# Optimization experiments

Hardware: AMD Instinct MI355X
Metric: run time of the kernel (lower is better)

## Reference

```python
import jax, jax.numpy as jnp
import numpy as np

D_MODEL = 1024
N_HEADS = 16
D_K = D_MODEL // N_HEADS
THETA = 10000.0
SEQ = 2048
BATCH = 2


def setup_inputs() -> dict:
    key = jax.random.key(0)
    ks = jax.random.split(key, 5)
    std = (2.0 / (D_MODEL + D_MODEL)) ** 0.5
    return {
        "x": jax.random.normal(ks[0], (BATCH, SEQ, D_MODEL), dtype=jnp.float32),
        "token_positions": jnp.arange(SEQ, dtype=jnp.int64 if jax.config.jax_enable_x64 else jnp.int32),
        "wq": jax.random.normal(ks[1], (D_MODEL, D_MODEL), dtype=jnp.float32) * std,
        "wk": jax.random.normal(ks[2], (D_MODEL, D_MODEL), dtype=jnp.float32) * std,
        "wv": jax.random.normal(ks[3], (D_MODEL, D_MODEL), dtype=jnp.float32) * std,
        "wo": jax.random.normal(ks[4], (D_MODEL, D_MODEL), dtype=jnp.float32) * std,
    }


def _apply_rope(t, token_positions):
    # t: [b, h, s, d_k]; interleaved even/odd rotation (RoPE)
    k = jnp.arange(D_K // 2, dtype=t.dtype)
    inv_freq = THETA ** (-2.0 * k / D_K)                     # [d_k/2]
    angles = token_positions.astype(t.dtype)[:, None] * inv_freq  # [s, d_k/2]
    cos, sin = jnp.cos(angles), jnp.sin(angles)
    even, odd = t[..., 0::2], t[..., 1::2]
    re = even * cos - odd * sin
    ro = odd * cos + even * sin
    # re-interleave: stack last then reshape back to [..., d_k]
    return jnp.stack([re, ro], axis=-1).reshape(t.shape)


def reference(x, token_positions, wq, wk, wv, wo):
    b, s, _ = x.shape
    def proj(w):
        y = jnp.einsum("bsd,ed->bse", x, w)               # Linear: x @ W^T
        return y.reshape(b, s, N_HEADS, D_K).transpose(0, 2, 1, 3)  # [b,h,s,dk]
    q, k, v = proj(wq), proj(wk), proj(wv)
    q = _apply_rope(q, token_positions)
    k = _apply_rope(k, token_positions)
    scores = jnp.einsum("bhqd,bhkd->bhqk", q, k) / jnp.sqrt(jnp.asarray(D_K, x.dtype))
    attn = jax.nn.softmax(scores, axis=-1)
    out = jnp.einsum("bhqk,bhkd->bhqd", attn, v)          # [b,h,s,dk]
    out = out.transpose(0, 2, 1, 3).reshape(b, s, D_MODEL)
    return jnp.einsum("bsd,ed->bse", out, wo)
```

## Files before the change

### kernel.cpp

```cpp
#include <hip/hip_runtime.h>
#include <stdint.h>

typedef __bf16 bf16x8 __attribute__((ext_vector_type(8)));
typedef __bf16 bf16x2 __attribute__((ext_vector_type(2)));
typedef float f32x4 __attribute__((ext_vector_type(4)));
typedef float f32x16 __attribute__((ext_vector_type(16)));
typedef unsigned short ushort_t;
typedef unsigned int uint;

#define SEQ    2048
#define DMODEL 1024
#define NHEAD  16
#define DKH    64
#define NBATCH 2
#define MROWS  (NBATCH*SEQ)
#define LOG2E  1.44269504088896340736f

__device__ __forceinline__ uint pk2(float a, float b) {
  bf16x2 t; t[0] = (__bf16)a; t[1] = (__bf16)b;
  return __builtin_bit_cast(uint, t);
}
__device__ __forceinline__ ushort_t b1(float a) {
  return __builtin_bit_cast(ushort_t, (__bf16)a);
}
__device__ __forceinline__ float fexp2(float x) {
#if __has_builtin(__builtin_amdgcn_exp2f)
  return __builtin_amdgcn_exp2f(x);
#else
  return exp2f(x);
#endif
}

__device__ __forceinline__ void gload16(const void* g, void* l) {
  __builtin_amdgcn_global_load_lds(
      (const __attribute__((address_space(1))) void*)g,
      (__attribute__((address_space(3))) void*)l, 16, 0, 0);
}

__device__ __forceinline__ f32x4 mfma16(bf16x8 a, bf16x8 b, f32x4 c) {
  return __builtin_amdgcn_mfma_f32_16x16x32_bf16(a, b, c, 0, 0, 0);
}
__device__ __forceinline__ f32x16 mfma32(bf16x8 a, bf16x8 b, f32x16 c) {
  return __builtin_amdgcn_mfma_f32_32x32x16_bf16(a, b, c, 0, 0, 0);
}

__global__ __launch_bounds__(256) void cvt_all(
    const float* __restrict__ x, const float* __restrict__ wq,
    const float* __restrict__ wk, const float* __restrict__ wv,
    const float* __restrict__ wo, uint2* __restrict__ out)
{
  int b = blockIdx.x;
  const float4* src; uint2* dst; int i;
  if (b < 4096) {
    i = b * 256 + threadIdx.x; src = (const float4*)x; dst = out;
  } else {
    int s = (b - 4096) >> 10;
    i = ((b - 4096) & 1023) * 256 + threadIdx.x;
    src = (const float4*)(s == 0 ? wq : s == 1 ? wk : s == 2 ? wv : wo);
    dst = out + (size_t)1048576 + (size_t)s * 262144;
  }
  float4 v = src[i];
  uint2 r; r.x = pk2(v.x, v.y); r.y = pk2(v.z, v.w);
  dst[i] = r;
}

__global__ __launch_bounds__(256) void rope_tab_kernel(const int* __restrict__ tokpos, float2* __restrict__ tab) {
  int t = blockIdx.x * 256 + threadIdx.x;
  int s = t >> 5, k = t & 31;
  double inv = pow(10000.0, -(double)(2 * k) / 64.0);
  double ang = (double)tokpos[s] * inv;
  tab[t] = make_float2((float)cos(ang), (float)sin(ang));
}

__global__ __launch_bounds__(256) void gemm_nt(
    const ushort_t* __restrict__ A, const ushort_t* __restrict__ W,
    const float2* __restrict__ tab,
    ushort_t* __restrict__ Qo, ushort_t* __restrict__ Ko, ushort_t* __restrict__ Vo,
    float* __restrict__ outf, int fused)
{
  __shared__ ushort_t lA[2][128 * 64];
  __shared__ ushort_t lB[2][128 * 64];
  const int tid = threadIdx.x;
  const int w = tid >> 6, l = tid & 63, lo = l & 15, hi = l >> 4;
  const int wr = (w >> 1) * 64, wc = (w & 1) * 64;
  const char* Ab = (const char*)A + (size_t)blockIdx.y * 128 * 2048;
  const char* Bb = (const char*)W + (size_t)blockIdx.x * 128 * 2048;
  f32x4 acc[4][4] = {};

  const int o0 = w * 1024 + l * 16;
  const int r0 = o0 >> 7;
  const int us = ((o0 >> 4) & 7) ^ (r0 & 7);
  const char* ap = Ab + (size_t)r0 * 2048 + us * 16;
  const char* bp = Bb + (size_t)r0 * 2048 + us * 16;

  auto stage = [&](char* dA, char* dB, const char* aq, const char* bq) {
    #pragma unroll
    for (int i = 0; i < 4; ++i) {
      gload16(aq + i * 65536, dA + w * 1024 + i * 4096);
      gload16(bq + i * 65536, dB + w * 1024 + i * 4096);
    }
  };
  auto comp = [&](const ushort_t* lAb, const ushort_t* lBb) {
    #pragma unroll
    for (int c = 0; c < 2; ++c) {
      bf16x8 af[4], wf[4];
      #pragma unroll
      for (int m = 0; m < 4; ++m) {
        int row = wr + m * 16 + lo;
        af[m] = *(const bf16x8*)((const char*)lAb + row * 128 + ((c * 64 + hi * 16) ^ ((row & 7) << 4)));
      }
      #pragma unroll
      for (int n = 0; n < 4; ++n) {
        int row = wc + n * 16 + lo;
        wf[n] = *(const bf16x8*)((const char*)lBb + row * 128 + ((c * 64 + hi * 16) ^ ((row & 7) << 4)));
      }
      #pragma unroll
      for (int m = 0; m < 4; ++m)
        #pragma unroll
        for (int n = 0; n < 4; ++n)
          acc[m][n] = mfma16(af[m], wf[n], acc[m][n]);
    }
  };

  stage((char*)lA[0], (char*)lB[0], ap, bp); ap += 128; bp += 128;
  __syncthreads();
  for (int it = 0; it < 16; it += 2) {
    stage((char*)lA[1], (char*)lB[1], ap, bp); ap += 128; bp += 128;
    comp(lA[0], lB[0]);
    __syncthreads();
    if (it + 2 < 16) { stage((char*)lA[0], (char*)lB[0], ap, bp); ap += 128; bp += 128; }
    comp(lA[1], lB[1]);
    __syncthreads();
  }

  const int mode = fused ? (blockIdx.x >> 3) : 3;
  const int colblk = fused ? (blockIdx.x & 7) : blockIdx.x;
  const int rowbase = blockIdx.y * 128 + wr + hi * 4;
  const int colbase = colblk * 128 + wc + lo;

  if (mode == 3) {
    #pragma unroll
    for (int m = 0; m < 4; ++m)
      #pragma unroll
      for (int n = 0; n < 4; ++n) {
        int e = colbase + n * 16;
        #pragma unroll
        for (int r = 0; r < 4; ++r) {
          int row = rowbase + m * 16 + r;
          outf[(size_t)row * 1024 + e] = acc[m][n][r];
        }
      }
    return;
  }
  if (mode == 2) {
    #pragma unroll
    for (int m = 0; m < 4; ++m) {
      int row0 = rowbase + m * 16;
      int b = row0 >> 11, s = row0 & 2047;
      #pragma unroll
      for (int n = 0; n < 4; ++n) {
        int e = colbase + n * 16;
        int h = e >> 6, dk = e & 63;
        uint2 pk;
        pk.x = pk2(acc[m][n][0], acc[m][n][1]);
        pk.y = pk2(acc[m][n][2], acc[m][n][3]);
        *(uint2*)(Vo + ((size_t)((b * NHEAD + h) * DKH + dk) * SEQ + s)) = pk;
      }
    }
    return;
  }
  ushort_t* outb = (mode == 0) ? Qo : Ko;
  const float qscale = (mode == 0) ? (0.125f * LOG2E) : 1.0f;
  #pragma unroll
  for (int m = 0; m < 4; ++m) {
    #pragma unroll
    for (int n = 0; n < 4; ++n) {
      int e = colbase + n * 16;
      int h = e >> 6, dk = e & 63, kf = dk >> 1;
      float sgn = (e & 1) ? 1.0f : -1.0f;
      #pragma unroll
      for (int r = 0; r < 4; ++r) {
        int row = rowbase + m * 16 + r;
        int s = row & 2047, b = row >> 11;
        float2 cs = tab[s * 32 + kf];
        float v = acc[m][n][r];
        float p = __shfl_xor(v, 1, 64);
        float res = (v * cs.x + sgn * p * cs.y) * qscale;
        outb[((size_t)((b * NHEAD + h) * SEQ + s)) * DKH + dk] = b1(res);
      }
    }
  }
}

__global__ __launch_bounds__(256) void attn_fwd(
    const ushort_t* __restrict__ Qg, const ushort_t* __restrict__ Kg,
    const ushort_t* __restrict__ VTg, ushort_t* __restrict__ attn)
{
  __shared__ char lds[49152];
  const int tid = threadIdx.x;
  const int w = tid >> 6, l = tid & 63;
  const int q31 = l & 31, hf = l >> 5, s7 = l & 7;
  const int bh = blockIdx.y;
  const int q0 = blockIdx.x * 128 + w * 32;
  const char* Kb = (const char*)Kg + (size_t)bh * 2048 * 128;
  const char* Vb = (const char*)VTg + (size_t)bh * 64 * 4096;

  bf16x8 qreg[4];
  {
    const ushort_t* qp = Qg + ((size_t)bh * 2048 + q0 + q31) * 64 + hf * 8;
    #pragma unroll
    for (int c = 0; c < 4; ++c) qreg[c] = *(const bf16x8*)(qp + c * 16);
  }

  f32x16 accO[2] = {{0,0,0,0,0,0,0,0,0,0,0,0,0,0,0,0},
                    {0,0,0,0,0,0,0,0,0,0,0,0,0,0,0,0}};
  float lsum = 0.f;

  const char* ra[4];
  #pragma unroll
  for (int c = 0; c < 4; ++c)
    ra[c] = lds + q31 * 128 + ((c * 32 + hf * 16) ^ (s7 << 4));
  const int lPoff = 32768 + w * 4096;
  char* wbase = lds + lPoff + q31 * 128 + hf * 8;

  const int o0 = tid * 16;
  const int r0 = o0 >> 7;
  const int us = ((o0 >> 4) & 7) ^ (r0 & 7);
  const char* kp = Kb + (size_t)r0 * 128 + us * 16;
  const char* vp = Vb + (size_t)r0 * 4096 + us * 16;

  auto stage = [&](char* base, const char* kq, const char* vq) {
    gload16(kq,          base + o0);
    gload16(kq + 4096,   base + 4096 + o0);
    gload16(vq,          base + 8192 + o0);
    gload16(vq + 131072, base + 12288 + o0);
  };

  auto tile = [&](int bo) {
    #pragma unroll
    for (int kb = 0; kb < 2; ++kb) {
      f32x16 s = {0,0,0,0,0,0,0,0,0,0,0,0,0,0,0,0};
      #pragma unroll
      for (int c = 0; c < 4; ++c) {
        bf16x8 kf = *(const bf16x8*)(ra[c] + bo + kb * 4096);
        s = mfma32(kf, qreg[c], s);
      }
      float p[16];
      float ts = 0.f;
      #pragma unroll
      for (int r = 0; r < 16; ++r) { p[r] = fexp2(s[r]); ts += p[r]; }
      lsum += ts;
      #pragma unroll
      for (int g2 = 0; g2 < 4; ++g2) {
        uint2 pk;
        pk.x = pk2(p[g2 * 4 + 0], p[g2 * 4 + 1]);
        pk.y = pk2(p[g2 * 4 + 2], p[g2 * 4 + 3]);
        *(uint2*)(wbase + ((kb * 64 + g2 * 16) ^ (s7 << 4))) = pk;
      }
      #pragma unroll
      for (int kcl = 0; kcl < 2; ++kcl) {
        int kc = kb * 2 + kcl;
        bf16x8 pb = *(const bf16x8*)(ra[kc] + lPoff);
        #pragma unroll
        for (int db = 0; db < 2; ++db) {
          bf16x8 vf = *(const bf16x8*)(ra[kc] + bo + 8192 + db * 4096);
          accO[db] = mfma32(vf, pb, accO[db]);
        }
      }
    }
  };

  stage(lds, kp, vp); kp += 8192; vp += 128;
  for (int kt = 0; kt < 32; kt += 2) {
    __syncthreads();
    stage(lds + 16384, kp, vp); kp += 8192; vp += 128;
    tile(0);
    __syncthreads();
    if (kt + 2 < 32) { stage(lds, kp, vp); kp += 8192; vp += 128; }
    tile(16384);
  }

  float lt = lsum + __shfl_xor(lsum, 32, 64);
  float inv = 1.0f / lt;
  int b = bh >> 4, head = bh & 15;
  ushort_t* op = attn + (size_t)(b * 2048 + q0 + q31) * 1024 + head * 64;
  #pragma unroll
  for (int db = 0; db < 2; ++db)
    #pragma unroll
    for (int m = 0; m < 4; ++m) {
      int d0 = db * 32 + m * 8 + hf * 4;
      uint2 pk;
      pk.x = pk2(accO[db][m * 4 + 0] * inv, accO[db][m * 4 + 1] * inv);
      pk.y = pk2(accO[db][m * 4 + 2] * inv, accO[db][m * 4 + 3] * inv);
      *(uint2*)(op + d0) = pk;
    }
}

extern "C" void kernel_launch(void* const* d_in, const int* in_sizes, int n_in,
                              void* d_out, int out_size, void* d_ws, size_t ws_size,
                              hipStream_t stream) {
  const float* x  = (const float*)d_in[0];
  const int* tok  = (const int*)d_in[1];
  const float* wq = (const float*)d_in[2];
  const float* wk = (const float*)d_in[3];
  const float* wv = (const float*)d_in[4];
  const float* wo = (const float*)d_in[5];
  float* out = (float*)d_out;
  char* ws = (char*)d_ws;

  size_t off = 0;
  float2* tab = (float2*)(ws + off); off += (size_t)SEQ * 32 * sizeof(float2);
  ushort_t* xb  = (ushort_t*)(ws + off); off += (size_t)MROWS * DMODEL * 2;
  ushort_t* wqkv = (ushort_t*)(ws + off); off += (size_t)3 * DMODEL * DMODEL * 2;
  ushort_t* wob = (ushort_t*)(ws + off); off += (size_t)DMODEL * DMODEL * 2;
  ushort_t* Qg  = (ushort_t*)(ws + off); off += (size_t)MROWS * DMODEL * 2;
  ushort_t* Kg  = (ushort_t*)(ws + off); off += (size_t)MROWS * DMODEL * 2;
  ushort_t* VTg = (ushort_t*)(ws + off); off += (size_t)MROWS * DMODEL * 2;
  ushort_t* attnb = xb;
  if (ws_size < off) return;

  cvt_all<<<8192, 256, 0, stream>>>(x, wq, wk, wv, wo, (uint2*)xb);
  rope_tab_kernel<<<256, 256, 0, stream>>>(tok, tab);

  gemm_nt<<<dim3(24, 32), 256, 0, stream>>>(xb, wqkv, tab, Qg, Kg, VTg, nullptr, 1);

  attn_fwd<<<dim3(SEQ / 128, NBATCH * NHEAD), 256, 0, stream>>>(Qg, Kg, VTg, attnb);

  gemm_nt<<<dim3(8, 32), 256, 0, stream>>>(attnb, wob, nullptr, nullptr, nullptr, nullptr, out, 0);
}
```

Measured before the change: 131.9 us.

## Process two 32-query blocks per wave in attention, halving waves per block

The attention kernel now runs 2 waves per block instead of 4, and each wave handles 64 query rows as two 32-row sub-blocks. The K and V fragments read from LDS are reused across both query sub-blocks, which cuts LDS read traffic per MFMA. The staging loop is rewritten so 128 threads fill the same 16 KB K/V tiles. In exchange, register pressure doubles for accumulators and Q fragments, and fewer waves per block may reduce latency hiding.

```diff
diff --git a/kernel.cpp b/kernel.cpp
--- a/kernel.cpp
+++ b/kernel.cpp
@@ -192,7 +192,7 @@
   }
 }
 
-__global__ __launch_bounds__(256) void attn_fwd(
+__global__ __launch_bounds__(128) void attn_fwd(
     const ushort_t* __restrict__ Qg, const ushort_t* __restrict__ Kg,
     const ushort_t* __restrict__ VTg, ushort_t* __restrict__ attn)
 {
@@ -201,70 +201,76 @@
   const int w = tid >> 6, l = tid & 63;
   const int q31 = l & 31, hf = l >> 5, s7 = l & 7;
   const int bh = blockIdx.y;
-  const int q0 = blockIdx.x * 128 + w * 32;
+  const int q0 = blockIdx.x * 128 + w * 64;
   const char* Kb = (const char*)Kg + (size_t)bh * 2048 * 128;
   const char* Vb = (const char*)VTg + (size_t)bh * 64 * 4096;
 
-  bf16x8 qreg[4];
-  {
-    const ushort_t* qp = Qg + ((size_t)bh * 2048 + q0 + q31) * 64 + hf * 8;
-    #pragma unroll
-    for (int c = 0; c < 4; ++c) qreg[c] = *(const bf16x8*)(qp + c * 16);
-  }
-
-  f32x16 accO[2] = {{0,0,0,0,0,0,0,0,0,0,0,0,0,0,0,0},
-                    {0,0,0,0,0,0,0,0,0,0,0,0,0,0,0,0}};
-  float lsum = 0.f;
+  bf16x8 qreg[2][4];
+  #pragma unroll
+  for (int qb = 0; qb < 2; ++qb) {
+    const ushort_t* qp = Qg + ((size_t)bh * 2048 + q0 + qb * 32 + q31) * 64 + hf * 8;
+    #pragma unroll
+    for (int c = 0; c < 4; ++c) qreg[qb][c] = *(const bf16x8*)(qp + c * 16);
+  }
+
+  f32x16 accO[2][2] = {};
+  float lsum[2] = {0.f, 0.f};
 
   const char* ra[4];
   #pragma unroll
   for (int c = 0; c < 4; ++c)
     ra[c] = lds + q31 * 128 + ((c * 32 + hf * 16) ^ (s7 << 4));
-  const int lPoff = 32768 + w * 4096;
+  const int lPoff = 32768 + w * 8192;
   char* wbase = lds + lPoff + q31 * 128 + hf * 8;
 
-  const int o0 = tid * 16;
-  const int r0 = o0 >> 7;
-  const int us = ((o0 >> 4) & 7) ^ (r0 & 7);
-  const char* kp = Kb + (size_t)r0 * 128 + us * 16;
-  const char* vp = Vb + (size_t)r0 * 4096 + us * 16;
+  const int su = (tid & 7) ^ ((tid >> 3) & 7);
+  const char* kp = Kb + (size_t)(tid >> 3) * 128 + su * 16;
+  const char* vp = Vb + (size_t)(tid >> 3) * 4096 + su * 16;
 
   auto stage = [&](char* base, const char* kq, const char* vq) {
-    gload16(kq,          base + o0);
-    gload16(kq + 4096,   base + 4096 + o0);
-    gload16(vq,          base + 8192 + o0);
-    gload16(vq + 131072, base + 12288 + o0);
+    #pragma unroll
+    for (int i = 0; i < 4; ++i)
+      gload16(kq + i * 2048, base + i * 2048 + tid * 16);
+    #pragma unroll
+    for (int i = 0; i < 4; ++i)
+      gload16(vq + i * 65536, base + 8192 + i * 2048 + tid * 16);
   };
 
   auto tile = [&](int bo) {
     #pragma unroll
     for (int kb = 0; kb < 2; ++kb) {
-      f32x16 s = {0,0,0,0,0,0,0,0,0,0,0,0,0,0,0,0};
-      #pragma unroll
-      for (int c = 0; c < 4; ++c) {
-        bf16x8 kf = *(const bf16x8*)(ra[c] + bo + kb * 4096);
-        s = mfma32(kf, qreg[c], s);
-      }
-      float p[16];
-      float ts = 0.f;
-      #pragma unroll
-      for (int r = 0; r < 16; ++r) { p[r] = fexp2(s[r]); ts += p[r]; }
-      lsum += ts;
-      #pragma unroll
-      for (int g2 = 0; g2 < 4; ++g2) {
-        uint2 pk;
-        pk.x = pk2(p[g2 * 4 + 0], p[g2 * 4 + 1]);
-        pk.y = pk2(p[g2 * 4 + 2], p[g2 * 4 + 3]);
-        *(uint2*)(wbase + ((kb * 64 + g2 * 16) ^ (s7 << 4))) = pk;
+      bf16x8 kf[4];
+      #pragma unroll
+      for (int c = 0; c < 4; ++c)
+        kf[c] = *(const bf16x8*)(ra[c] + bo + kb * 4096);
+      #pragma unroll
+      for (int qb = 0; qb < 2; ++qb) {
+        f32x16 s = {};
+        #pragma unroll
+        for (int c = 0; c < 4; ++c) s = mfma32(kf[c], qreg[qb][c], s);
+        float p[16];
+        float ts = 0.f;
+        #pragma unroll
+        for (int r = 0; r < 16; ++r) { p[r] = fexp2(s[r]); ts += p[r]; }
+        lsum[qb] += ts;
+        #pragma unroll
+        for (int g2 = 0; g2 < 4; ++g2) {
+          uint2 pk;
+          pk.x = pk2(p[g2 * 4 + 0], p[g2 * 4 + 1]);
+          pk.y = pk2(p[g2 * 4 + 2], p[g2 * 4 + 3]);
+          *(uint2*)(wbase + qb * 4096 + ((kb * 64 + g2 * 16) ^ (s7 << 4))) = pk;
+        }
       }
       #pragma unroll
       for (int kcl = 0; kcl < 2; ++kcl) {
         int kc = kb * 2 + kcl;
-        bf16x8 pb = *(const bf16x8*)(ra[kc] + lPoff);
-        #pragma unroll
-        for (int db = 0; db < 2; ++db) {
-          bf16x8 vf = *(const bf16x8*)(ra[kc] + bo + 8192 + db * 4096);
-          accO[db] = mfma32(vf, pb, accO[db]);
+        bf16x8 vf0 = *(const bf16x8*)(ra[kc] + bo + 8192);
+        bf16x8 vf1 = *(const bf16x8*)(ra[kc] + bo + 8192 + 4096);
+        #pragma unroll
+        for (int qb = 0; qb < 2; ++qb) {
+          bf16x8 pb = *(const bf16x8*)(ra[kc] + lPoff + qb * 4096);
+          accO[qb][0] = mfma32(vf0, pb, accO[qb][0]);
+          accO[qb][1] = mfma32(vf1, pb, accO[qb][1]);
         }
       }
     }
@@ -280,20 +286,23 @@
     tile(16384);
   }
 
-  float lt = lsum + __shfl_xor(lsum, 32, 64);
-  float inv = 1.0f / lt;
   int b = bh >> 4, head = bh & 15;
-  ushort_t* op = attn + (size_t)(b * 2048 + q0 + q31) * 1024 + head * 64;
   #pragma unroll
-  for (int db = 0; db < 2; ++db)
-    #pragma unroll
-    for (int m = 0; m < 4; ++m) {
-      int d0 = db * 32 + m * 8 + hf * 4;
-      uint2 pk;
-      pk.x = pk2(accO[db][m * 4 + 0] * inv, accO[db][m * 4 + 1] * inv);
-      pk.y = pk2(accO[db][m * 4 + 2] * inv, accO[db][m * 4 + 3] * inv);
-      *(uint2*)(op + d0) = pk;
-    }
+  for (int qb = 0; qb < 2; ++qb) {
+    float lt = lsum[qb] + __shfl_xor(lsum[qb], 32, 64);
+    float inv = 1.0f / lt;
+    ushort_t* op = attn + (size_t)(b * 2048 + q0 + qb * 32 + q31) * 1024 + head * 64;
+    #pragma unroll
+    for (int db = 0; db < 2; ++db)
+      #pragma unroll
+      for (int m = 0; m < 4; ++m) {
+        int d0 = db * 32 + m * 8 + hf * 4;
+        uint2 pk;
+        pk.x = pk2(accO[qb][db][m * 4 + 0] * inv, accO[qb][db][m * 4 + 1] * inv);
+        pk.y = pk2(accO[qb][db][m * 4 + 2] * inv, accO[qb][db][m * 4 + 3] * inv);
+        *(uint2*)(op + d0) = pk;
+      }
+  }
 }
 
 extern "C" void kernel_launch(void* const* d_in, const int* in_sizes, int n_in,
@@ -324,7 +333,7 @@
 
   gemm_nt<<<dim3(24, 32), 256, 0, stream>>>(xb, wqkv, tab, Qg, Kg, VTg, nullptr, 1);
 
-  attn_fwd<<<dim3(SEQ / 128, NBATCH * NHEAD), 256, 0, stream>>>(Qg, Kg, VTg, attnb);
+  attn_fwd<<<dim3(SEQ / 128, NBATCH * NHEAD), 128, 0, stream>>>(Qg, Kg, VTg, attnb);
 
   gemm_nt<<<dim3(8, 32), 256, 0, stream>>>(attnb, wob, nullptr, nullptr, nullptr, nullptr, out, 0);
 }
```

Measured after the change: 134.3 us. No clear change (+1.8%).
